# Performance work log

Measured on AMD Instinct MI355X. Metric: run time of the kernel, lower is better.

## Reference

```python
import jax, jax.numpy as jnp
import numpy as np

B, T, U, D, V = 4, 256, 128, 512, 1024

def setup_inputs() -> dict:
    key = jax.random.key(0)
    k1, k2, k3, k4, k5, k6 = jax.random.split(key, 6)
    return {
        "source_encodings": jax.random.normal(k1, (B, T, D), dtype=jnp.float32),
        "source_lengths": jax.random.randint(k2, (B,), 1, T + 1, dtype=jnp.int32),
        "target_encodings": jax.random.normal(k3, (B, U, D), dtype=jnp.float32),
        "target_lengths": jax.random.randint(k4, (B,), 1, U + 1, dtype=jnp.int32),
        "W": jax.random.normal(k5, (V, D), dtype=jnp.float32) * (1.0 / np.sqrt(D)),
        "b": jax.random.normal(k6, (V,), dtype=jnp.float32) * 0.01,
    }

def reference(source_encodings, source_lengths, target_encodings, target_lengths, W, b):
    # broadcast add: (B,T,1,D) + (B,1,U,D) -> (B,T,U,D)
    joint = source_encodings[:, :, None, :] + target_encodings[:, None, :, :]
    act = jax.nn.relu(joint)
    # linear: (B,T,U,D) @ (D,V) + b -> (B,T,U,V)
    out = jnp.einsum("btud,vd->btuv", act, W) + b
    return out, source_lengths, target_lengths
```

## Files before the change

kernel.cpp:

```cpp
#include <hip/hip_runtime.h>


typedef __attribute__((ext_vector_type(4))) float f32x4;
typedef __attribute__((ext_vector_type(8))) __bf16 bf16x8;
typedef __attribute__((ext_vector_type(8))) unsigned short u16x8;

#define BM 128
#define BN 128
#define BK 64
#define KDIM 512
#define VDIM 1024
#define MROWS 131072
#define OUT_MAIN 134217728ull

__device__ __forceinline__ unsigned short f2bf(float f) {
    unsigned u = __float_as_uint(f);
    unsigned r = 0x7fffu + ((u >> 16) & 1u);
    return (unsigned short)((u + r) >> 16);
}

__global__ __launch_bounds__(256) void prep_act(const float* __restrict__ src,
                                                const float* __restrict__ tgt,
                                                unsigned short* __restrict__ act) {
    int idx = blockIdx.x * 256 + threadIdx.x;
    int m   = idx >> 6;
    int kk  = (idx & 63) << 3;
    int u   = m & 127;
    int bt  = m >> 7;
    int b   = bt >> 8;
    const float* sp = src + ((size_t)bt << 9) + kk;
    const float* tp = tgt + ((((size_t)b << 7) + u) << 9) + kk;
    f32x4 s0 = *(const f32x4*)sp;
    f32x4 s1 = *(const f32x4*)(sp + 4);
    f32x4 t0 = *(const f32x4*)tp;
    f32x4 t1 = *(const f32x4*)(tp + 4);
    u16x8 r;
#pragma unroll
    for (int j = 0; j < 4; j++) {
        float a = s0[j] + t0[j]; a = a > 0.f ? a : 0.f;
        float c = s1[j] + t1[j]; c = c > 0.f ? c : 0.f;
        r[j]     = f2bf(a);
        r[j + 4] = f2bf(c);
    }
    *(u16x8*)(act + ((size_t)m << 9) + kk) = r;
}

__global__ __launch_bounds__(256) void prep_w(const float* __restrict__ W,
                                              unsigned short* __restrict__ Wb,
                                              const int* __restrict__ slen,
                                              const int* __restrict__ tlen,
                                              float* __restrict__ tail) {
    int idx = blockIdx.x * 256 + threadIdx.x;
    const float* wp = W + ((size_t)idx << 3);
    f32x4 w0 = *(const f32x4*)wp;
    f32x4 w1 = *(const f32x4*)(wp + 4);
    u16x8 r;
#pragma unroll
    for (int j = 0; j < 4; j++) { r[j] = f2bf(w0[j]); r[j + 4] = f2bf(w1[j]); }
    *(u16x8*)(Wb + ((size_t)idx << 3)) = r;
    if (idx < 4)      tail[idx] = (float)slen[idx];
    else if (idx < 8) tail[idx] = (float)tlen[idx - 4];
}

__global__ __launch_bounds__(256) void gemm_bf16(const unsigned short* __restrict__ A,
                                                 const unsigned short* __restrict__ Bw,
                                                 const float* __restrict__ bias,
                                                 float* __restrict__ out) {
    __shared__ __align__(16) unsigned short As[BM * BK];
    __shared__ __align__(16) unsigned short Bs[BN * BK];

    const int tid  = threadIdx.x;
    const int bid  = blockIdx.x;
    const int mt   = bid >> 3;
    const int nt   = bid & 7;
    const int m0   = mt * BM;
    const int n0   = nt * BN;

    const int lane = tid & 63;
    const int wid  = tid >> 6;
    const int wr   = wid >> 1;
    const int wc   = wid & 1;

    const int srow = tid >> 3;
    const int scol = (tid & 7) * 8;

    f32x4 acc[4][4];
#pragma unroll
    for (int i = 0; i < 4; i++)
#pragma unroll
        for (int j = 0; j < 4; j++) acc[i][j] = (f32x4)0.f;

    const unsigned short* Ag = A  + (size_t)m0 * KDIM + scol;
    const unsigned short* Bg = Bw + (size_t)n0 * KDIM + scol;

    for (int k0 = 0; k0 < KDIM; k0 += BK) {
#pragma unroll
        for (int i = 0; i < 4; i++) {
            int r = srow + i * 32;
            __builtin_amdgcn_global_load_lds(
                (const __attribute__((address_space(1))) void*)(Ag + (size_t)r * KDIM + k0),
                (__attribute__((address_space(3))) void*)(&As[r * BK + scol]), 16, 0, 0);
        }
#pragma unroll
        for (int i = 0; i < 4; i++) {
            int r = srow + i * 32;
            __builtin_amdgcn_global_load_lds(
                (const __attribute__((address_space(1))) void*)(Bg + (size_t)r * KDIM + k0),
                (__attribute__((address_space(3))) void*)(&Bs[r * BK + scol]), 16, 0, 0);
        }
        __syncthreads();

#pragma unroll
        for (int kk = 0; kk < 2; kk++) {
            bf16x8 af[4], bf[4];
            const int klo = kk * 32 + (lane >> 4) * 8;
#pragma unroll
            for (int mi = 0; mi < 4; mi++) {
                int row = wr * 64 + mi * 16 + (lane & 15);
                af[mi] = *(const bf16x8*)&As[row * BK + klo];
            }
#pragma unroll
            for (int ni = 0; ni < 4; ni++) {
                int col = wc * 64 + ni * 16 + (lane & 15);
                bf[ni] = *(const bf16x8*)&Bs[col * BK + klo];
            }
#pragma unroll
            for (int mi = 0; mi < 4; mi++)
#pragma unroll
                for (int ni = 0; ni < 4; ni++)
                    acc[mi][ni] = __builtin_amdgcn_mfma_f32_16x16x32_bf16(
                        af[mi], bf[ni], acc[mi][ni], 0, 0, 0);
        }
        __syncthreads();
    }

#pragma unroll
    for (int ni = 0; ni < 4; ni++) {
        int col = n0 + wc * 64 + ni * 16 + (lane & 15);
        float bv = bias[col];
#pragma unroll
        for (int mi = 0; mi < 4; mi++) {
            int rbase = m0 + wr * 64 + mi * 16 + ((lane >> 4) << 2);
#pragma unroll
            for (int i = 0; i < 4; i++) {
                out[(size_t)(rbase + i) * VDIM + col] = acc[mi][ni][i] + bv;
            }
        }
    }
}

extern "C" void kernel_launch(void* const* d_in, const int* in_sizes, int n_in,
                              void* d_out, int out_size, void* d_ws, size_t ws_size,
                              hipStream_t stream) {
    const float* src  = (const float*)d_in[0];
    const int*   slen = (const int*)d_in[1];
    const float* tgt  = (const float*)d_in[2];
    const int*   tlen = (const int*)d_in[3];
    const float* W    = (const float*)d_in[4];
    const float* bias = (const float*)d_in[5];
    float* out = (float*)d_out;

    unsigned short* act = (unsigned short*)d_ws;
    unsigned short* Wb  = (unsigned short*)((char*)d_ws + OUT_MAIN);

    prep_act<<<32768, 256, 0, stream>>>(src, tgt, act);
    prep_w<<<256, 256, 0, stream>>>(W, Wb, slen, tlen, out + OUT_MAIN);
    gemm_bf16<<<8192, 256, 0, stream>>>(act, Wb, bias, out);
}
```

Before: 761.0 us.

## Fuse broadcast-add/ReLU activation build into GEMM with LDS-resident A tile

Removes the separate prep_act kernel, which wrote a 128 MB bf16 activation tensor to global memory that the GEMM then read back. Each 512-thread block now owns one (b,t) row of 128 u values. It builds the full 128x512 bf16 activation tile in LDS with an XOR swizzle, then loops over all 8 N tiles, streaming W through a double-buffered LDS slice. The cost is about 160 KB of LDS per block, which leaves one block per CU, plus a smaller per-wave accumulator tile and a barrier every K step.

```diff
diff --git a/kernel.cpp b/kernel.cpp
--- a/kernel.cpp
+++ b/kernel.cpp
@@ -5,44 +5,15 @@
 typedef __attribute__((ext_vector_type(8))) __bf16 bf16x8;
 typedef __attribute__((ext_vector_type(8))) unsigned short u16x8;
 
-#define BM 128
-#define BN 128
-#define BK 64
 #define KDIM 512
 #define VDIM 1024
-#define MROWS 131072
+#define BK 64
 #define OUT_MAIN 134217728ull
 
 __device__ __forceinline__ unsigned short f2bf(float f) {
     unsigned u = __float_as_uint(f);
     unsigned r = 0x7fffu + ((u >> 16) & 1u);
     return (unsigned short)((u + r) >> 16);
-}
-
-__global__ __launch_bounds__(256) void prep_act(const float* __restrict__ src,
-                                                const float* __restrict__ tgt,
-                                                unsigned short* __restrict__ act) {
-    int idx = blockIdx.x * 256 + threadIdx.x;
-    int m   = idx >> 6;
-    int kk  = (idx & 63) << 3;
-    int u   = m & 127;
-    int bt  = m >> 7;
-    int b   = bt >> 8;
-    const float* sp = src + ((size_t)bt << 9) + kk;
-    const float* tp = tgt + ((((size_t)b << 7) + u) << 9) + kk;
-    f32x4 s0 = *(const f32x4*)sp;
-    f32x4 s1 = *(const f32x4*)(sp + 4);
-    f32x4 t0 = *(const f32x4*)tp;
-    f32x4 t1 = *(const f32x4*)(tp + 4);
-    u16x8 r;
-#pragma unroll
-    for (int j = 0; j < 4; j++) {
-        float a = s0[j] + t0[j]; a = a > 0.f ? a : 0.f;
-        float c = s1[j] + t1[j]; c = c > 0.f ? c : 0.f;
-        r[j]     = f2bf(a);
-        r[j + 4] = f2bf(c);
-    }
-    *(u16x8*)(act + ((size_t)m << 9) + kk) = r;
 }
 
 __global__ __launch_bounds__(256) void prep_w(const float* __restrict__ W,
@@ -62,90 +33,123 @@
     else if (idx < 8) tail[idx] = (float)tlen[idx - 4];
 }
 
-__global__ __launch_bounds__(256) void gemm_bf16(const unsigned short* __restrict__ A,
-                                                 const unsigned short* __restrict__ Bw,
-                                                 const float* __restrict__ bias,
-                                                 float* __restrict__ out) {
-    __shared__ __align__(16) unsigned short As[BM * BK];
-    __shared__ __align__(16) unsigned short Bs[BN * BK];
+__global__ __launch_bounds__(512, 1) void joiner_fused(
+    const float* __restrict__ src, const float* __restrict__ tgt,
+    const unsigned short* __restrict__ Wb, const float* __restrict__ bias,
+    float* __restrict__ out)
+{
+    __shared__ __align__(16) unsigned short As[128 * KDIM];
+    __shared__ __align__(16) unsigned short Bs[2][128 * BK];
 
-    const int tid  = threadIdx.x;
-    const int bid  = blockIdx.x;
-    const int mt   = bid >> 3;
-    const int nt   = bid & 7;
-    const int m0   = mt * BM;
-    const int n0   = nt * BN;
+    const int tid = threadIdx.x;
+    const int bt  = blockIdx.x;
+    const int b   = bt >> 8;
+
+    const int scol = tid >> 3;
+    const int skb  = (tid & 7) * 8;
+
+    __builtin_amdgcn_global_load_lds(
+        (const __attribute__((address_space(1))) void*)(Wb + (size_t)scol * KDIM + skb),
+        (__attribute__((address_space(3))) void*)(&Bs[0][scol * BK + skb]), 16, 0, 0);
+    __builtin_amdgcn_global_load_lds(
+        (const __attribute__((address_space(1))) void*)(Wb + (size_t)(64 + scol) * KDIM + skb),
+        (__attribute__((address_space(3))) void*)(&Bs[0][(64 + scol) * BK + skb]), 16, 0, 0);
+
+    {
+        const int r = tid >> 2;
+        const int q = tid & 3;
+        const float* sp = src + (size_t)bt * KDIM + q * 128;
+        const float* tp = tgt + (size_t)(b * 128 + r) * KDIM + q * 128;
+        const int rx = (r & 7) << 3;
+#pragma unroll
+        for (int ch = 0; ch < 16; ++ch) {
+            f32x4 s0 = *(const f32x4*)(sp + ch * 8);
+            f32x4 s1 = *(const f32x4*)(sp + ch * 8 + 4);
+            f32x4 t0 = *(const f32x4*)(tp + ch * 8);
+            f32x4 t1 = *(const f32x4*)(tp + ch * 8 + 4);
+            u16x8 v;
+#pragma unroll
+            for (int j = 0; j < 4; j++) {
+                float a = s0[j] + t0[j]; a = a > 0.f ? a : 0.f;
+                float c = s1[j] + t1[j]; c = c > 0.f ? c : 0.f;
+                v[j]     = f2bf(a);
+                v[j + 4] = f2bf(c);
+            }
+            int k0 = q * 128 + ch * 8;
+            *(u16x8*)&As[r * KDIM + (k0 ^ rx)] = v;
+        }
+    }
+    __syncthreads();
 
     const int lane = tid & 63;
     const int wid  = tid >> 6;
     const int wr   = wid >> 1;
     const int wc   = wid & 1;
+    const int l15  = lane & 15;
+    const int lq   = lane >> 4;
 
-    const int srow = tid >> 3;
-    const int scol = (tid & 7) * 8;
+    f32x4 acc[2][4];
+#pragma unroll
+    for (int mi = 0; mi < 2; mi++)
+#pragma unroll
+        for (int ni = 0; ni < 4; ni++) acc[mi][ni] = (f32x4)0.f;
 
-    f32x4 acc[4][4];
-#pragma unroll
-    for (int i = 0; i < 4; i++)
-#pragma unroll
-        for (int j = 0; j < 4; j++) acc[i][j] = (f32x4)0.f;
+    for (int ci = 0; ci < 64; ++ci) {
+        const int buf = ci & 1;
+        const int nt  = ci >> 3;
+        const int ks  = ci & 7;
 
-    const unsigned short* Ag = A  + (size_t)m0 * KDIM + scol;
-    const unsigned short* Bg = Bw + (size_t)n0 * KDIM + scol;
-
-    for (int k0 = 0; k0 < KDIM; k0 += BK) {
-#pragma unroll
-        for (int i = 0; i < 4; i++) {
-            int r = srow + i * 32;
+        if (ci + 1 < 64) {
+            const int nn = (ci + 1) >> 3;
+            const int nk = ((ci + 1) & 7) * BK;
+            const unsigned short* bg = Wb + (size_t)(nn * 128) * KDIM + nk + skb;
             __builtin_amdgcn_global_load_lds(
-                (const __attribute__((address_space(1))) void*)(Ag + (size_t)r * KDIM + k0),
-                (__attribute__((address_space(3))) void*)(&As[r * BK + scol]), 16, 0, 0);
+                (const __attribute__((address_space(1))) void*)(bg + (size_t)scol * KDIM),
+                (__attribute__((address_space(3))) void*)(&Bs[buf ^ 1][scol * BK + skb]), 16, 0, 0);
+            __builtin_amdgcn_global_load_lds(
+                (const __attribute__((address_space(1))) void*)(bg + (size_t)(64 + scol) * KDIM),
+                (__attribute__((address_space(3))) void*)(&Bs[buf ^ 1][(64 + scol) * BK + skb]), 16, 0, 0);
         }
-#pragma unroll
-        for (int i = 0; i < 4; i++) {
-            int r = srow + i * 32;
-            __builtin_amdgcn_global_load_lds(
-                (const __attribute__((address_space(1))) void*)(Bg + (size_t)r * KDIM + k0),
-                (__attribute__((address_space(3))) void*)(&Bs[r * BK + scol]), 16, 0, 0);
-        }
-        __syncthreads();
 
 #pragma unroll
-        for (int kk = 0; kk < 2; kk++) {
-            bf16x8 af[4], bf[4];
-            const int klo = kk * 32 + (lane >> 4) * 8;
+        for (int kk = 0; kk < 2; ++kk) {
+            bf16x8 af[2], bf[4];
+            const int klo  = ks * BK + kk * 32 + lq * 8;
+            const int kloB = kk * 32 + lq * 8;
 #pragma unroll
-            for (int mi = 0; mi < 4; mi++) {
-                int row = wr * 64 + mi * 16 + (lane & 15);
-                af[mi] = *(const bf16x8*)&As[row * BK + klo];
+            for (int mi = 0; mi < 2; mi++) {
+                int row = wr * 32 + mi * 16 + l15;
+                af[mi] = *(const bf16x8*)&As[row * KDIM + (klo ^ ((row & 7) << 3))];
             }
 #pragma unroll
             for (int ni = 0; ni < 4; ni++) {
-                int col = wc * 64 + ni * 16 + (lane & 15);
-                bf[ni] = *(const bf16x8*)&Bs[col * BK + klo];
+                int col = wc * 64 + ni * 16 + l15;
+                bf[ni] = *(const bf16x8*)&Bs[buf][col * BK + kloB];
             }
 #pragma unroll
-            for (int mi = 0; mi < 4; mi++)
+            for (int mi = 0; mi < 2; mi++)
 #pragma unroll
                 for (int ni = 0; ni < 4; ni++)
                     acc[mi][ni] = __builtin_amdgcn_mfma_f32_16x16x32_bf16(
                         af[mi], bf[ni], acc[mi][ni], 0, 0, 0);
         }
-        __syncthreads();
-    }
 
+        if (ks == 7) {
 #pragma unroll
-    for (int ni = 0; ni < 4; ni++) {
-        int col = n0 + wc * 64 + ni * 16 + (lane & 15);
-        float bv = bias[col];
+            for (int ni = 0; ni < 4; ni++) {
+                int col = nt * 128 + wc * 64 + ni * 16 + l15;
+                float bv = bias[col];
 #pragma unroll
-        for (int mi = 0; mi < 4; mi++) {
-            int rbase = m0 + wr * 64 + mi * 16 + ((lane >> 4) << 2);
+                for (int mi = 0; mi < 2; mi++) {
+                    int rbase = bt * 128 + wr * 32 + mi * 16 + lq * 4;
 #pragma unroll
-            for (int i = 0; i < 4; i++) {
-                out[(size_t)(rbase + i) * VDIM + col] = acc[mi][ni][i] + bv;
+                    for (int i = 0; i < 4; i++)
+                        out[(size_t)(rbase + i) * VDIM + col] = acc[mi][ni][i] + bv;
+                    acc[mi][ni] = (f32x4)0.f;
+                }
             }
         }
+        __syncthreads();
     }
 }
 
@@ -160,10 +164,8 @@
     const float* bias = (const float*)d_in[5];
     float* out = (float*)d_out;
 
-    unsigned short* act = (unsigned short*)d_ws;
-    unsigned short* Wb  = (unsigned short*)((char*)d_ws + OUT_MAIN);
+    unsigned short* Wb = (unsigned short*)d_ws;
 
-    prep_act<<<32768, 256, 0, stream>>>(src, tgt, act);
     prep_w<<<256, 256, 0, stream>>>(W, Wb, slen, tlen, out + OUT_MAIN);
-    gemm_bf16<<<8192, 256, 0, stream>>>(act, Wb, bias, out);
+    joiner_fused<<<1024, 512, 0, stream>>>(src, tgt, Wb, bias, out);
 }
```

After: 821.1 us. +7.9%, slower.
